# Performance work log

Hardware: AMD Instinct MI355X
Metric: run time of the kernel (lower is better)

## Reference

```python
import jax, jax.numpy as jnp
import numpy as np

B, S, D = 4, 2048, 1024

def setup_inputs() -> dict:
    key = jax.random.key(0)
    k1, k2, k3, k4 = jax.random.split(key, 4)
    scale = 1.0 / np.sqrt(D)
    token_encodings = jax.random.normal(k1, (B, S, D), dtype=jnp.float32)
    W_q = jax.random.normal(k2, (D, D), dtype=jnp.float32) * scale
    W_k = jax.random.normal(k3, (D, D), dtype=jnp.float32) * scale
    W_v = jax.random.normal(k4, (D, D), dtype=jnp.float32) * scale
    # causal mask, broadcastable to (B, S, S); 0 means masked
    mask = jnp.tril(jnp.ones((S, S), dtype=jnp.int32))[None, :, :]
    return {"token_encodings": token_encodings, "mask": mask,
            "W_q": W_q, "W_k": W_k, "W_v": W_v}

def reference(token_encodings, mask, W_q, W_k, W_v):
    # nn.Linear(d, d, bias=False): y = x @ W.T
    q = jnp.einsum('bsd,ed->bse', token_encodings, W_q)
    k = jnp.einsum('bsd,ed->bse', token_encodings, W_k)
    v = jnp.einsum('bsd,ed->bse', token_encodings, W_v)
    d_k = q.shape[-1]
    scores = jnp.einsum('bqd,bkd->bqk', q, k) / jnp.sqrt(jnp.asarray(d_k, q.dtype))
    scores = jnp.where(mask == 0, jnp.asarray(-jnp.inf, scores.dtype), scores)
    attn_weights = jax.nn.softmax(scores, axis=-1)
    output = jnp.einsum('bqk,bkd->bqd', attn_weights, v)
    return (output, attn_weights)
```

## Files before the change

kernel.cpp:

```cpp
#include <hip/hip_runtime.h>
#include <hip/hip_bf16.h>
#include <stdint.h>
#include <math.h>


typedef __hip_bfloat16 bf16;
typedef __attribute__((ext_vector_type(8))) short short8;
typedef __attribute__((ext_vector_type(4))) float f32x4;

#define BM 128
#define BN 128
#define BK 64

static constexpr int Bb = 4;
static constexpr int S  = 2048;
static constexpr int D  = 1024;
static constexpr size_t QK_ELEMS = (size_t)Bb * S * D;
static constexpr size_t SS_ELEMS = (size_t)S * S;
static constexpr size_t W_ELEMS  = (size_t)D * D;

__device__ __forceinline__ void async16(const bf16* g, bf16* l) {
  __builtin_amdgcn_global_load_lds(
      (__attribute__((address_space(1))) const void*)g,
      (__attribute__((address_space(3))) void*)l, 16, 0, 0);
}

template<bool SWAP>
__device__ __forceinline__ void gemm_core(const bf16* __restrict__ A,
                                          const bf16* __restrict__ B,
                                          int ldA, int ldB, int ksteps,
                                          bf16* As, bf16* Bs,
                                          f32x4 acc[4][4])
{
  const int tid  = threadIdx.x;
  const int lane = tid & 63;
  const int wave = tid >> 6;
  const int wm   = (wave & 1) * 64;
  const int wn   = (wave >> 1) * 64;
  const int m16  = lane & 15;
  const int kq   = lane >> 4;
  const int sw   = m16 & 7;

  int r[4], f[4];
  #pragma unroll
  for (int i = 0; i < 4; ++i) {
    const int c = tid + i * 256;
    r[i] = c >> 3;
    f[i] = (((c & 7) ^ (r[i] & 7))) * 8;
  }

  for (int ks = 0; ks < ksteps; ++ks) {
    const int k = ks * BK;
    #pragma unroll
    for (int i = 0; i < 4; ++i)
      async16(A + (size_t)r[i] * ldA + k + f[i], As + ((size_t)tid + i * 256) * 8);
    #pragma unroll
    for (int i = 0; i < 4; ++i)
      async16(B + (size_t)r[i] * ldB + k + f[i], Bs + ((size_t)tid + i * 256) * 8);
    __syncthreads();

    #pragma unroll
    for (int j = 0; j < 2; ++j) {
      const int jc = j * 4 + kq;
      const int sl = jc ^ sw;
      short8 af[4], bfr[4];
      #pragma unroll
      for (int i = 0; i < 4; ++i)
        af[i] = *(const short8*)&As[((wm + i * 16 + m16) * 8 + sl) * 8];
      #pragma unroll
      for (int i = 0; i < 4; ++i)
        bfr[i] = *(const short8*)&Bs[((wn + i * 16 + m16) * 8 + sl) * 8];

      #pragma unroll
      for (int mi = 0; mi < 4; ++mi) {
        #pragma unroll
        for (int ni = 0; ni < 4; ++ni) {
          if (SWAP)
            acc[mi][ni] = __builtin_amdgcn_mfma_f32_16x16x32_bf16(
                bfr[ni], af[mi], acc[mi][ni], 0, 0, 0);
          else
            acc[mi][ni] = __builtin_amdgcn_mfma_f32_16x16x32_bf16(
                af[mi], bfr[ni], acc[mi][ni], 0, 0, 0);
        }
      }
    }
    __syncthreads();
  }
}

__device__ __forceinline__ void zero_acc(f32x4 acc[4][4]) {
  #pragma unroll
  for (int mi = 0; mi < 4; ++mi)
    #pragma unroll
    for (int ni = 0; ni < 4; ++ni)
      acc[mi][ni] = (f32x4){0.f, 0.f, 0.f, 0.f};
}

__device__ __forceinline__ unsigned short f2b(float f) {
  __hip_bfloat16 h = __float2bfloat16(f);
  return *(unsigned short*)&h;
}

__global__ __launch_bounds__(256)
void cvt_kernel(const float* __restrict__ X,  const float* __restrict__ Wq,
                const float* __restrict__ Wk, const float* __restrict__ Wv,
                bf16* __restrict__ Xb, bf16* __restrict__ Wqb,
                bf16* __restrict__ Wkb, bf16* __restrict__ Wvb)
{
  const size_t g = ((size_t)blockIdx.x * 256 + threadIdx.x) * 4;
  const float* src; bf16* dst; size_t off;
  if (g < QK_ELEMS) { src = X; dst = Xb; off = g; }
  else {
    const size_t h = g - QK_ELEMS;
    const int w = (int)(h >> 20);
    off = h & (W_ELEMS - 1);
    src = (w == 0) ? Wq : (w == 1) ? Wk : Wv;
    dst = (w == 0) ? Wqb : (w == 1) ? Wkb : Wvb;
  }
  const float4 v = *(const float4*)(src + off);
  uint2 o;
  o.x = (uint32_t)f2b(v.x) | ((uint32_t)f2b(v.y) << 16);
  o.y = (uint32_t)f2b(v.z) | ((uint32_t)f2b(v.w) << 16);
  *(uint2*)((unsigned short*)dst + off) = o;
}

__global__ __launch_bounds__(256, 4)
void qkv_kernel(const bf16* __restrict__ X, const bf16* __restrict__ Wq,
                const bf16* __restrict__ Wk, const bf16* __restrict__ Wv,
                bf16* __restrict__ Q, bf16* __restrict__ Ko,
                bf16* __restrict__ Vt)
{
  __shared__ __align__(16) bf16 As[BM * BK];
  __shared__ __align__(16) bf16 Bs[BN * BK];
  const int L = blockIdx.x;
  const int x = L & 7;
  const int s = L >> 3;
  const int nt  = s & 7;
  const int zmt = ((s >> 3) << 3) | x;
  const int z   = zmt >> 6;
  const int mt  = zmt & 63;
  const bf16* W = (z == 0) ? Wq : (z == 1) ? Wk : Wv;

  const int lane = threadIdx.x & 63, wave = threadIdx.x >> 6;
  const int wm = (wave & 1) * 64, wn = (wave >> 1) * 64;
  const int col0 = lane & 15, row0 = (lane >> 4) * 4;

  f32x4 acc[4][4];
  zero_acc(acc);
  if (z < 2) {
    gemm_core<false>(X + (size_t)mt * 128 * D, W + (size_t)nt * 128 * D,
                     D, D, D / BK, As, Bs, acc);
    bf16* Out = z ? Ko : Q;
    #pragma unroll
    for (int mi = 0; mi < 4; ++mi)
      #pragma unroll
      for (int ni = 0; ni < 4; ++ni)
        #pragma unroll
        for (int r = 0; r < 4; ++r) {
          const int grow = mt * 128 + wm + mi * 16 + row0 + r;
          const int gcol = nt * 128 + wn + ni * 16 + col0;
          Out[(size_t)grow * D + gcol] = __float2bfloat16(acc[mi][ni][r]);
        }
  } else {
    gemm_core<true>(X + (size_t)mt * 128 * D, W + (size_t)nt * 128 * D,
                    D, D, D / BK, As, Bs, acc);
    const int b = (mt * 128) >> 11;
    #pragma unroll
    for (int mi = 0; mi < 4; ++mi)
      #pragma unroll
      for (int ni = 0; ni < 4; ++ni)
        #pragma unroll
        for (int r = 0; r < 4; ++r) {
          const int ge = nt * 128 + wn + ni * 16 + row0 + r;
          const int gs = mt * 128 + wm + mi * 16 + col0;
          const int sl = gs & (S - 1);
          Vt[(size_t)b * D * S + (size_t)ge * S + sl] = __float2bfloat16(acc[mi][ni][r]);
        }
  }
}

__global__ __launch_bounds__(256, 4)
void scores_kernel(const bf16* __restrict__ Q, const bf16* __restrict__ K,
                   float* __restrict__ Sc)
{
  const int t = blockIdx.x, b = blockIdx.y;
  int qt = (int)((sqrtf(8.f * (float)t + 1.f) - 1.f) * 0.5f);
  while ((qt + 1) * (qt + 2) / 2 <= t) ++qt;
  while (qt * (qt + 1) / 2 > t) --qt;
  const int kt = t - qt * (qt + 1) / 2;

  __shared__ __align__(16) bf16 As[BM * BK];
  __shared__ __align__(16) bf16 Bs[BN * BK];

  f32x4 acc[4][4];
  zero_acc(acc);
  gemm_core<false>(Q + ((size_t)b * S + qt * 128) * D,
                   K + ((size_t)b * S + kt * 128) * D,
                   D, D, D / BK, As, Bs, acc);

  const int lane = threadIdx.x & 63, wave = threadIdx.x >> 6;
  const int wm = (wave & 1) * 64, wn = (wave >> 1) * 64;
  const int col0 = lane & 15, row0 = (lane >> 4) * 4;
  float* out = Sc + (size_t)b * SS_ELEMS;
  #pragma unroll
  for (int mi = 0; mi < 4; ++mi)
    #pragma unroll
    for (int ni = 0; ni < 4; ++ni)
      #pragma unroll
      for (int r = 0; r < 4; ++r) {
        const int gq = qt * 128 + wm + mi * 16 + row0 + r;
        const int gk = kt * 128 + wn + ni * 16 + col0;
        out[(size_t)gq * S + gk] = acc[mi][ni][r] * 0.03125f;
      }
}

__device__ __forceinline__ float wave_max(float v) {
  #pragma unroll
  for (int o = 32; o > 0; o >>= 1) v = fmaxf(v, __shfl_xor(v, o, 64));
  return v;
}
__device__ __forceinline__ float wave_sum(float v) {
  #pragma unroll
  for (int o = 32; o > 0; o >>= 1) v += __shfl_xor(v, o, 64);
  return v;
}

__global__ __launch_bounds__(256)
void softmax_kernel(float* __restrict__ Attn, bf16* __restrict__ Pb)
{
  const int row = blockIdx.x;
  const int b = row >> 11, i = row & (S - 1);
  float* s = Attn + (size_t)b * SS_ELEMS + (size_t)i * S;
  bf16* p  = Pb   + (size_t)b * SS_ELEMS + (size_t)i * S;
  const int t = threadIdx.x;
  const int lane = t & 63, wave = t >> 6;
  __shared__ float red[4];

  float4 v[2];
  #pragma unroll
  for (int u = 0; u < 2; ++u) {
    const int base = (t + u * 256) * 4;
    if (base + 3 <= i) {
      v[u] = *(const float4*)(s + base);
    } else if (base > i) {
      v[u] = make_float4(-INFINITY, -INFINITY, -INFINITY, -INFINITY);
    } else {
      v[u].x = (base + 0 <= i) ? s[base + 0] : -INFINITY;
      v[u].y = (base + 1 <= i) ? s[base + 1] : -INFINITY;
      v[u].z = (base + 2 <= i) ? s[base + 2] : -INFINITY;
      v[u].w = (base + 3 <= i) ? s[base + 3] : -INFINITY;
    }
  }

  float m = -INFINITY;
  #pragma unroll
  for (int u = 0; u < 2; ++u)
    m = fmaxf(m, fmaxf(fmaxf(v[u].x, v[u].y), fmaxf(v[u].z, v[u].w)));
  m = wave_max(m);
  if (lane == 0) red[wave] = m;
  __syncthreads();
  m = fmaxf(fmaxf(red[0], red[1]), fmaxf(red[2], red[3]));
  __syncthreads();

  float sum = 0.f;
  #pragma unroll
  for (int u = 0; u < 2; ++u) {
    v[u].x = __expf(v[u].x - m); sum += v[u].x;
    v[u].y = __expf(v[u].y - m); sum += v[u].y;
    v[u].z = __expf(v[u].z - m); sum += v[u].z;
    v[u].w = __expf(v[u].w - m); sum += v[u].w;
  }
  sum = wave_sum(sum);
  if (lane == 0) red[wave] = sum;
  __syncthreads();
  sum = red[0] + red[1] + red[2] + red[3];
  const float inv = 1.f / sum;

  const int dt_end = ((i >> 7) + 1) * 128;
  #pragma unroll
  for (int u = 0; u < 2; ++u) {
    const int base = (t + u * 256) * 4;
    float4 w;
    w.x = v[u].x * inv; w.y = v[u].y * inv;
    w.z = v[u].z * inv; w.w = v[u].w * inv;
    *(float4*)(s + base) = w;
    if (base < dt_end) {
      ushort4 pk;
      pk.x = f2b(w.x); pk.y = f2b(w.y); pk.z = f2b(w.z); pk.w = f2b(w.w);
      *(ushort4*)((unsigned short*)p + base) = pk;
    }
  }
}

__global__ __launch_bounds__(256, 4)
void out_kernel(const bf16* __restrict__ P, const bf16* __restrict__ Vt,
                float* __restrict__ O)
{
  const int L = blockIdx.x;
  const int x = L & 7;
  const int s = L >> 3;
  const int dt  = s & 7;
  const int qtb = ((s >> 3) << 3) | x;
  const int qt  = 15 - (qtb >> 2);
  const int b   = qtb & 3;

  __shared__ __align__(16) bf16 As[BM * BK];
  __shared__ __align__(16) bf16 Bs[BN * BK];

  f32x4 acc[4][4];
  zero_acc(acc);
  const int ksteps = (qt + 1) * (128 / BK);
  gemm_core<false>(P + (size_t)b * SS_ELEMS + (size_t)qt * 128 * S,
                   Vt + (size_t)b * D * S + (size_t)dt * 128 * S,
                   S, S, ksteps, As, Bs, acc);

  const int lane = threadIdx.x & 63, wave = threadIdx.x >> 6;
  const int wm = (wave & 1) * 64, wn = (wave >> 1) * 64;
  const int col0 = lane & 15, row0 = (lane >> 4) * 4;
  #pragma unroll
  for (int mi = 0; mi < 4; ++mi)
    #pragma unroll
    for (int ni = 0; ni < 4; ++ni)
      #pragma unroll
      for (int r = 0; r < 4; ++r) {
        const int gq = qt * 128 + wm + mi * 16 + row0 + r;
        const int gd = dt * 128 + wn + ni * 16 + col0;
        O[((size_t)b * S + gq) * D + gd] = acc[mi][ni][r];
      }
}

extern "C" void kernel_launch(void* const* d_in, const int* in_sizes, int n_in,
                              void* d_out, int out_size, void* d_ws, size_t ws_size,
                              hipStream_t stream) {
  const float* X  = (const float*)d_in[0];
  const float* Wq = (const float*)d_in[2];
  const float* Wk = (const float*)d_in[3];
  const float* Wv = (const float*)d_in[4];

  float* Out  = (float*)d_out;
  float* Attn = Out + QK_ELEMS;

  bf16* Q   = (bf16*)d_ws;
  bf16* K   = Q + QK_ELEMS;
  bf16* Vt  = K + QK_ELEMS;
  bf16* Xb  = Vt + QK_ELEMS;
  bf16* Wqb = Xb + QK_ELEMS;
  bf16* Wkb = Wqb + W_ELEMS;
  bf16* Wvb = Wkb + W_ELEMS;
  bf16* Pb  = (bf16*)d_ws;

  const int cvt_blocks = (int)((QK_ELEMS + 3 * W_ELEMS) / 4 / 256);
  cvt_kernel<<<cvt_blocks, 256, 0, stream>>>(X, Wq, Wk, Wv, Xb, Wqb, Wkb, Wvb);
  qkv_kernel<<<dim3(1536), 256, 0, stream>>>(Xb, Wqb, Wkb, Wvb, Q, K, Vt);
  const int ntile = (S / 128) * (S / 128 + 1) / 2;
  scores_kernel<<<dim3(ntile, Bb), 256, 0, stream>>>(Q, K, Attn);
  softmax_kernel<<<dim3(Bb * S), 256, 0, stream>>>(Attn, Pb);
  out_kernel<<<dim3(512), 256, 0, stream>>>(Pb, Vt, Out);
}
```

Baseline: 281.6 us.

## Use 64x128 tiles for scores and PV GEMMs with finer causal bounds

Adds a 64-row by 128-column GEMM core and switches the scores and output kernels to 64-row query tiles, which doubles the block count. The output kernel now stops its K loop at the 64-row causal boundary, skipping the half-tile of zero probabilities the 128-row tiles processed. This aims to cut wasted causal work and improve load balance and occupancy. In exchange, each tile has lower arithmetic intensity and more global and LDS traffic per FLOP.

```diff
diff --git a/kernel.cpp b/kernel.cpp
--- a/kernel.cpp
+++ b/kernel.cpp
@@ -96,6 +96,75 @@
       acc[mi][ni] = (f32x4){0.f, 0.f, 0.f, 0.f};
 }
 
+__device__ __forceinline__ void gemm_core64(const bf16* __restrict__ A,
+                                            const bf16* __restrict__ B,
+                                            int ldA, int ldB, int ksteps,
+                                            bf16* As, bf16* Bs,
+                                            f32x4 acc[4][2])
+{
+  const int tid  = threadIdx.x;
+  const int lane = tid & 63;
+  const int wave = tid >> 6;
+  const int wn   = wave * 32;
+  const int m16  = lane & 15;
+  const int kq   = lane >> 4;
+  const int sw   = m16 & 7;
+
+  int ra[2], fa[2], rb[4], fb[4];
+  #pragma unroll
+  for (int i = 0; i < 2; ++i) {
+    const int c = tid + i * 256;
+    ra[i] = c >> 3;
+    fa[i] = ((c & 7) ^ (ra[i] & 7)) * 8;
+  }
+  #pragma unroll
+  for (int i = 0; i < 4; ++i) {
+    const int c = tid + i * 256;
+    rb[i] = c >> 3;
+    fb[i] = ((c & 7) ^ (rb[i] & 7)) * 8;
+  }
+
+  for (int ks = 0; ks < ksteps; ++ks) {
+    const int k = ks * BK;
+    #pragma unroll
+    for (int i = 0; i < 2; ++i)
+      async16(A + (size_t)ra[i] * ldA + k + fa[i], As + ((size_t)tid + i * 256) * 8);
+    #pragma unroll
+    for (int i = 0; i < 4; ++i)
+      async16(B + (size_t)rb[i] * ldB + k + fb[i], Bs + ((size_t)tid + i * 256) * 8);
+    __syncthreads();
+
+    #pragma unroll
+    for (int j = 0; j < 2; ++j) {
+      const int jc = j * 4 + kq;
+      const int sl = jc ^ sw;
+      short8 af[4], bfr[2];
+      #pragma unroll
+      for (int i = 0; i < 4; ++i)
+        af[i] = *(const short8*)&As[((i * 16 + m16) * 8 + sl) * 8];
+      #pragma unroll
+      for (int i = 0; i < 2; ++i)
+        bfr[i] = *(const short8*)&Bs[((wn + i * 16 + m16) * 8 + sl) * 8];
+
+      #pragma unroll
+      for (int mi = 0; mi < 4; ++mi)
+        #pragma unroll
+        for (int ni = 0; ni < 2; ++ni)
+          acc[mi][ni] = __builtin_amdgcn_mfma_f32_16x16x32_bf16(
+              af[mi], bfr[ni], acc[mi][ni], 0, 0, 0);
+    }
+    __syncthreads();
+  }
+}
+
+__device__ __forceinline__ void zero_acc64(f32x4 acc[4][2]) {
+  #pragma unroll
+  for (int mi = 0; mi < 4; ++mi)
+    #pragma unroll
+    for (int ni = 0; ni < 2; ++ni)
+      acc[mi][ni] = (f32x4){0.f, 0.f, 0.f, 0.f};
+}
+
 __device__ __forceinline__ unsigned short f2b(float f) {
   __hip_bfloat16 h = __float2bfloat16(f);
   return *(unsigned short*)&h;
@@ -184,32 +253,33 @@
                    float* __restrict__ Sc)
 {
   const int t = blockIdx.x, b = blockIdx.y;
-  int qt = (int)((sqrtf(8.f * (float)t + 1.f) - 1.f) * 0.5f);
-  while ((qt + 1) * (qt + 2) / 2 <= t) ++qt;
-  while (qt * (qt + 1) / 2 > t) --qt;
-  const int kt = t - qt * (qt + 1) / 2;
-
-  __shared__ __align__(16) bf16 As[BM * BK];
-  __shared__ __align__(16) bf16 Bs[BN * BK];
-
-  f32x4 acc[4][4];
-  zero_acc(acc);
-  gemm_core<false>(Q + ((size_t)b * S + qt * 128) * D,
-                   K + ((size_t)b * S + kt * 128) * D,
-                   D, D, D / BK, As, Bs, acc);
+  int m = (int)((sqrtf(4.f * (float)t + 1.f) - 1.f) * 0.5f);
+  while ((m + 1) * (m + 2) <= t) ++m;
+  while (m * (m + 1) > t) --m;
+  const int r_ = t - m * (m + 1);
+  const int qi = 2 * m + (r_ > m ? 1 : 0);
+  const int kt = (r_ > m) ? (r_ - (m + 1)) : r_;
+
+  __shared__ __align__(16) bf16 As[64 * BK];
+  __shared__ __align__(16) bf16 Bs[128 * BK];
+
+  f32x4 acc[4][2];
+  zero_acc64(acc);
+  gemm_core64(Q + ((size_t)b * S + qi * 64) * D,
+              K + ((size_t)b * S + kt * 128) * D,
+              D, D, D / BK, As, Bs, acc);
 
   const int lane = threadIdx.x & 63, wave = threadIdx.x >> 6;
-  const int wm = (wave & 1) * 64, wn = (wave >> 1) * 64;
   const int col0 = lane & 15, row0 = (lane >> 4) * 4;
   float* out = Sc + (size_t)b * SS_ELEMS;
   #pragma unroll
   for (int mi = 0; mi < 4; ++mi)
     #pragma unroll
-    for (int ni = 0; ni < 4; ++ni)
+    for (int ni = 0; ni < 2; ++ni)
       #pragma unroll
       for (int r = 0; r < 4; ++r) {
-        const int gq = qt * 128 + wm + mi * 16 + row0 + r;
-        const int gk = kt * 128 + wn + ni * 16 + col0;
+        const int gq = qi * 64 + mi * 16 + row0 + r;
+        const int gk = kt * 128 + wave * 32 + ni * 16 + col0;
         out[(size_t)gq * S + gk] = acc[mi][ni][r] * 0.03125f;
       }
 }
@@ -300,31 +370,29 @@
   const int x = L & 7;
   const int s = L >> 3;
   const int dt  = s & 7;
-  const int qtb = ((s >> 3) << 3) | x;
-  const int qt  = 15 - (qtb >> 2);
-  const int b   = qtb & 3;
-
-  __shared__ __align__(16) bf16 As[BM * BK];
-  __shared__ __align__(16) bf16 Bs[BN * BK];
-
-  f32x4 acc[4][4];
-  zero_acc(acc);
-  const int ksteps = (qt + 1) * (128 / BK);
-  gemm_core<false>(P + (size_t)b * SS_ELEMS + (size_t)qt * 128 * S,
-                   Vt + (size_t)b * D * S + (size_t)dt * 128 * S,
-                   S, S, ksteps, As, Bs, acc);
+  const int qb  = ((s >> 3) << 3) | x;
+  const int Qi  = 31 - (qb >> 2);
+  const int b   = qb & 3;
+
+  __shared__ __align__(16) bf16 As[64 * BK];
+  __shared__ __align__(16) bf16 Bs[128 * BK];
+
+  f32x4 acc[4][2];
+  zero_acc64(acc);
+  gemm_core64(P + (size_t)b * SS_ELEMS + (size_t)Qi * 64 * S,
+              Vt + (size_t)b * D * S + (size_t)dt * 128 * S,
+              S, S, Qi + 1, As, Bs, acc);
 
   const int lane = threadIdx.x & 63, wave = threadIdx.x >> 6;
-  const int wm = (wave & 1) * 64, wn = (wave >> 1) * 64;
   const int col0 = lane & 15, row0 = (lane >> 4) * 4;
   #pragma unroll
   for (int mi = 0; mi < 4; ++mi)
     #pragma unroll
-    for (int ni = 0; ni < 4; ++ni)
+    for (int ni = 0; ni < 2; ++ni)
       #pragma unroll
       for (int r = 0; r < 4; ++r) {
-        const int gq = qt * 128 + wm + mi * 16 + row0 + r;
-        const int gd = dt * 128 + wn + ni * 16 + col0;
+        const int gq = Qi * 64 + mi * 16 + row0 + r;
+        const int gd = dt * 128 + wave * 32 + ni * 16 + col0;
         O[((size_t)b * S + gq) * D + gd] = acc[mi][ni][r];
       }
 }
@@ -352,8 +420,8 @@
   const int cvt_blocks = (int)((QK_ELEMS + 3 * W_ELEMS) / 4 / 256);
   cvt_kernel<<<cvt_blocks, 256, 0, stream>>>(X, Wq, Wk, Wv, Xb, Wqb, Wkb, Wvb);
   qkv_kernel<<<dim3(1536), 256, 0, stream>>>(Xb, Wqb, Wkb, Wvb, Q, K, Vt);
-  const int ntile = (S / 128) * (S / 128 + 1) / 2;
-  scores_kernel<<<dim3(ntile, Bb), 256, 0, stream>>>(Q, K, Attn);
+  const int ntile64 = 2 * (S / 128) * (S / 128 + 1) / 2;
+  scores_kernel<<<dim3(ntile64, Bb), 256, 0, stream>>>(Q, K, Attn);
   softmax_kernel<<<dim3(Bb * S), 256, 0, stream>>>(Attn, Pb);
-  out_kernel<<<dim3(512), 256, 0, stream>>>(Pb, Vt, Out);
-}
+  out_kernel<<<dim3(1024), 256, 0, stream>>>(Pb, Vt, Out);
+}
```

Measured after the change: 267.1 us. 5.1% less time.
